# Kernel tuning notes

Hardware: AMD Instinct MI355X
Metric: run time of the kernel (lower is better)

## Reference

```python
import jax, jax.numpy as jnp
import numpy as np
from jax import lax

B, C, H, W = 16, 256, 80, 80
MID = 64
BN_EPS = 1e-5

SOBEL_X = jnp.array([[-1., 0., 1.], [-2., 0., 2.], [-1., 0., 1.]], jnp.float32) / 8.0
SOBEL_Y = jnp.array([[-1., -2., -1.], [0., 0., 0.], [1., 2., 1.]], jnp.float32) / 8.0
HAAR_LH = jnp.array([[1., -1.], [1., -1.]], jnp.float32) / 2.0
HAAR_HL = jnp.array([[1., 1.], [-1., -1.]], jnp.float32) / 2.0

DN = ('NCHW', 'OIHW', 'NCHW')

def dwconv(x, k2d, pad):
    # depthwise conv: same 2d kernel applied to every channel independently
    c = x.shape[1]
    k = jnp.broadcast_to(k2d[None, None], (c, 1) + k2d.shape)
    return lax.conv_general_dilated(x, k, (1, 1), [(pad, pad), (pad, pad)],
                                    dimension_numbers=DN, feature_group_count=c)

def avg_pool5(x):
    # matches F.avg_pool2d(k=5, s=1, p=2) with count_include_pad=True (divide by 25 always)
    s = lax.reduce_window(x, 0.0, lax.add, (1, 1, 5, 5), (1, 1, 1, 1),
                          [(0, 0), (0, 0), (2, 2), (2, 2)])
    return s / 25.0

def local_variance(x):
    m = avg_pool5(x)
    msq = avg_pool5(x * x)
    return jnp.clip(msq - m * m, 0.0, None)

def bn_silu(x, g, b, m, v):
    # inference batchnorm + SiLU, per-channel params over dim 1
    scale = (g / jnp.sqrt(v + BN_EPS))[None, :, None, None]
    shift = (b - m * g / jnp.sqrt(v + BN_EPS))[None, :, None, None]
    return jax.nn.silu(x * scale + shift)

def setup_inputs() -> dict:
    key = jax.random.key(0)
    ks = jax.random.split(key, 12)
    return {
        'x': jax.random.normal(ks[0], (B, C, H, W), jnp.float32),
        'proj_w': jax.random.normal(ks[1], (MID, C), jnp.float32) * 0.05,
        'bn1_g': jax.random.uniform(ks[2], (MID,), jnp.float32),
        'bn1_b': jax.random.normal(ks[3], (MID,), jnp.float32) * 0.1,
        'bn1_m': jax.random.normal(ks[4], (MID,), jnp.float32) * 0.1,
        'bn1_v': jax.random.uniform(ks[5], (MID,), jnp.float32) + 0.5,
        'fuse1_w': jax.random.normal(ks[6], (MID, MID + 2, 3, 3), jnp.float32) * 0.05,
        'bn2_g': jax.random.uniform(ks[7], (MID,), jnp.float32),
        'bn2_b': jax.random.normal(ks[8], (MID,), jnp.float32) * 0.1,
        'bn2_m': jax.random.normal(ks[9], (MID,), jnp.float32) * 0.1,
        'bn2_v': jax.random.uniform(ks[10], (MID,), jnp.float32) + 0.5,
        'fuse2_w': jax.random.normal(ks[11], (1, MID), jnp.float32) * 0.1,
    }

def reference(x, proj_w, bn1_g, bn1_b, bn1_m, bn1_v,
              fuse1_w, bn2_g, bn2_b, bn2_m, bn2_v, fuse2_w):
    b, c, h, w = x.shape
    # --- edge density ---
    gx = dwconv(x, SOBEL_X, 1)
    gy = dwconv(x, SOBEL_Y, 1)
    edge = jnp.sqrt(gx * gx + gy * gy).mean(axis=1, keepdims=True)  # (B,1,H,W)
    edge_density = edge / (avg_pool5(edge) + 1e-6)
    # --- periodicity ---
    lh = dwconv(x, HAAR_LH, 0)  # (B,C,H-1,W-1)
    hl = dwconv(x, HAAR_HL, 0)
    lh = jax.image.resize(lh, (b, c, h, w), method='bilinear')  # half-pixel, matches align_corners=False
    hl = jax.image.resize(hl, (b, c, h, w), method='bilinear')
    period = jnp.sqrt(local_variance(lh) + local_variance(hl) + 1e-6).mean(axis=1, keepdims=True)
    # --- feat_proj: 1x1 conv + BN + SiLU ---
    feat = bn_silu(jnp.einsum('bchw,mc->bmhw', x, proj_w), bn1_g, bn1_b, bn1_m, bn1_v)
    # --- fuse: 3x3 conv + BN + SiLU -> 1x1 conv -> sigmoid ---
    combined = jnp.concatenate([feat, edge_density, period], axis=1)  # (B,MID+2,H,W)
    y = lax.conv_general_dilated(combined, fuse1_w, (1, 1), [(1, 1), (1, 1)], dimension_numbers=DN)
    y = bn_silu(y, bn2_g, bn2_b, bn2_m, bn2_v)
    weight = jax.nn.sigmoid(jnp.einsum('bmhw,om->bohw', y, fuse2_w))  # (B,1,H,W)
    return x * weight
```

## Files before the change

### kernel.cpp

```cpp
#include <hip/hip_runtime.h>
#include <hip/hip_bf16.h>
#include <math.h>

#define HWN 6400
#define CC 256
#define MIDN 64

typedef _Float16 f16x8 __attribute__((ext_vector_type(8)));
typedef _Float16 f16x4 __attribute__((ext_vector_type(4)));
typedef _Float16 h2    __attribute__((ext_vector_type(2)));
typedef float    f32x4 __attribute__((ext_vector_type(4)));
typedef int      i32x4 __attribute__((ext_vector_type(4)));
typedef unsigned short u16;

__device__ __forceinline__ h2 pk2(float a, float b) {
    return __builtin_bit_cast(h2, __builtin_amdgcn_cvt_pkrtz(a, b));
}
__device__ __forceinline__ float h2lo(h2 v) { return (float)v[0]; }
__device__ __forceinline__ float h2hi(h2 v) { return (float)v[1]; }
__device__ __forceinline__ unsigned h2u(h2 v) { return __builtin_bit_cast(unsigned, v); }
__device__ __forceinline__ h2 u2h(unsigned u) { return __builtin_bit_cast(h2, u); }
__device__ __forceinline__ float u16f(u16 v) { return (float)__builtin_bit_cast(_Float16, v); }
__device__ __forceinline__ float vsqrtf_(float x) { float r; asm("v_sqrt_f32 %0, %1" : "=v"(r) : "v"(x)); return r; }

__global__ void prep_kernel(const float* __restrict__ proj_w,
                            const float* __restrict__ g1, const float* __restrict__ b1,
                            const float* __restrict__ m1, const float* __restrict__ v1,
                            const float* __restrict__ f1w,
                            const float* __restrict__ g2, const float* __restrict__ b2,
                            const float* __restrict__ m2, const float* __restrict__ v2,
                            _Float16* __restrict__ apack_proj,
                            _Float16* __restrict__ apack_fuse,
                            float* __restrict__ bias1, float* __restrict__ bias2) {
    int gid = blockIdx.x * blockDim.x + threadIdx.x;
    int stride = gridDim.x * blockDim.x;
    if (gid < MIDN) {
        float s1 = g1[gid] * rsqrtf(v1[gid] + 1e-5f);
        bias1[gid] = b1[gid] - m1[gid] * s1;
        float s2 = g2[gid] * rsqrtf(v2[gid] + 1e-5f);
        bias2[gid] = b2[gid] - m2[gid] * s2;
    }
    for (int i = gid; i < 8 * 4 * 64 * 8; i += stride) {
        int j = i & 7, lane = (i >> 3) & 63, w = (i >> 9) & 3, c = i >> 11;
        int m = w * 16 + (lane & 15);
        int ch = c * 32 + (lane >> 4) * 8 + j;
        float s1 = g1[m] * rsqrtf(v1[m] + 1e-5f);
        apack_proj[i] = (_Float16)(proj_w[m * CC + ch] * s1);
    }
    for (int i = gid; i < 9 * 3 * 4 * 64 * 8; i += stride) {
        int j = i & 7, lane = (i >> 3) & 63, w = (i >> 9) & 3;
        int tc = i >> 11; int c = tc % 3, t = tc / 3;
        int m = w * 16 + (lane & 15);
        int ch = c * 32 + (lane >> 4) * 8 + j;
        float s2 = g2[m] * rsqrtf(v2[m] + 1e-5f);
        float v = 0.f;
        if (ch < 66) v = f1w[(m * 66 + ch) * 9 + t] * s2;
        apack_fuse[i] = (_Float16)v;
    }
}

__launch_bounds__(256, 4)
__global__ void edge_period_pc_kernel(const float* __restrict__ x,
                                      u16* __restrict__ part_e,
                                      u16* __restrict__ part_p) {
    __shared__ unsigned wb[4][88];
    volatile unsigned (*wbv)[88] = wb;
    int tid = threadIdx.x;
    int w = tid >> 6, l = tid & 63;
    int b = blockIdx.y, cg = blockIdx.x;
    int row0 = w * 20;
    int im1 = (l + 63) & 63, ip1 = (l + 1) & 63;
    bool is0 = (l == 0), is63 = (l == 63), isB = (l < 16);

    if (l < 4) wbv[w][(l < 2) ? l : 80 + l] = 0u;

    float cwA = (l <= 0) ? 1.f : ((l >= 79) ? 0.f : (0.99375f - 0.0125f * (float)l));
    int cB = 64 + l;
    float cwB = (cB >= 79) ? 0.f : (0.99375f - 0.0125f * (float)cB);
    h2 v_pk = pk2(0.5f * cwA, 0.5f * cwB);
    h2 u_pk = pk2(0.5f * (1.f - cwA), 0.5f * (1.f - cwB));

    const float* xch = x + ((size_t)(b * CC + cg)) * HWN;
    u16* pe = part_e + ((size_t)(cg * 16 + b)) * HWN;
    u16* pp = part_p + ((size_t)(cg * 16 + b)) * HWN;

    auto rawload = [&](int rr) -> h2 {
        float a = 0.f, bb = 0.f;
        if (rr >= 0 && rr < 80) {
            a = xch[rr * 80 + l];
            if (isB) bb = xch[rr * 80 + 64 + l];
        }
        return pk2(a, bb);
    };
    auto mktrip = [&](h2 xc, h2& t0, h2& t2) {
        int xi = __builtin_bit_cast(int, xc);
        unsigned um = (unsigned)__shfl(xi, im1);
        unsigned up = (unsigned)__shfl(xi, ip1);
        um = is0 ? ((um & 0xFFFFu) << 16) : um;
        up = is63 ? (up >> 16) : up;
        t0 = u2h(um); t2 = u2h(up);
    };
    h2 xm1_0, xm1_1, xm1_2, x0_0, x0_1, x0_2, xp1_0, xp1_1, xp1_2;
    h2 rh, nh;
    nh = rawload(row0 - 3);
    rh = rawload(row0 - 2);
    xm1_1 = nh; mktrip(nh, xm1_0, xm1_2);
    x0_1 = rh;  mktrip(rh, x0_0, x0_2);
    rh = rawload(row0 - 1);
    h2 lhc_p, hlc_p;
    {
        h2 sa = xm1_0 + x0_0, sb = xm1_1 + x0_1, sc2 = xm1_2 + x0_2;
        h2 da = xm1_0 - x0_0, db = xm1_1 - x0_1, dc = xm1_2 - x0_2;
        lhc_p = u_pk * (sa - sb) + v_pk * (sb - sc2);
        hlc_p = u_pk * (da + db) + v_pk * (db + dc);
    }
    h2 ringA[5], ringB[5], ringS[5];
#pragma unroll
    for (int s = 0; s < 24; s++) {
        int r = row0 - 2 + s;
        if (s < 23) nh = rawload(row0 + s);
        xp1_1 = rh; mktrip(rh, xp1_0, xp1_2);
        if (s >= 2 && s < 22) {
            h2 gx = (xm1_2 - xm1_0) + (x0_2 - x0_0) + (x0_2 - x0_0) + (xp1_2 - xp1_0);
            h2 gy = (xp1_0 - xm1_0) + (xp1_1 - xm1_1) + (xp1_1 - xm1_1) + (xp1_2 - xm1_2);
            h2 g2v = gx * gx + gy * gy;
            unsigned eu = h2u(pk2(vsqrtf_(h2lo(g2v)) * 0.125f, vsqrtf_(h2hi(g2v)) * 0.125f));
            pe[r * 80 + l] = (u16)(eu & 0xFFFFu);
            if (isB) pe[r * 80 + 64 + l] = (u16)(eu >> 16);
        }
        h2 sa = x0_0 + xp1_0, sb = x0_1 + xp1_1, sc2 = x0_2 + xp1_2;
        h2 da = x0_0 - xp1_0, db = x0_1 - xp1_1, dc = x0_2 - xp1_2;
        h2 lhc = u_pk * (sa - sb) + v_pk * (sb - sc2);
        h2 hlc = u_pk * (da + db) + v_pk * (db + dc);
        float cw = (r <= 0) ? 1.f : ((r >= 79) ? 0.f : (0.99375f - 0.0125f * (float)r));
        h2 cwp = pk2(cw, cw), pwp = pk2(1.f - cw, 1.f - cw);
        h2 lhr = pwp * lhc_p + cwp * lhc;
        h2 hlr = pwp * hlc_p + cwp * hlc;
        lhc_p = lhc; hlc_p = hlc;
        unsigned lu = h2u(lhr), hu = h2u(hlr);
        unsigned fA = (lu & 0xFFFFu) | (hu << 16);
        unsigned fB = (lu >> 16) | (hu & 0xFFFF0000u);
        bool fv = (r >= 0) && (r < 80);
        if (!fv) { fA = 0u; fB = 0u; }
        wbv[w][2 + l] = fA;
        if (isB) wbv[w][66 + l] = fB;
        unsigned am2 = wbv[w][l], am1 = wbv[w][l + 1], ap1 = wbv[w][l + 3], ap2 = wbv[w][l + 4];
        unsigned bm2 = 0, bm1 = 0, bp1 = 0, bp2 = 0;
        if (isB) { bm2 = wbv[w][64 + l]; bm1 = wbv[w][65 + l]; bp1 = wbv[w][67 + l]; bp2 = wbv[w][68 + l]; }
        h2 fAh = u2h(fA), fBh = u2h(fB);
        h2 n0 = u2h(am2), n1 = u2h(am1), n2 = u2h(ap1), n3 = u2h(ap2);
        h2 hA = fAh + n0 + n1 + n2 + n3;
        h2 qa = fAh * fAh + n0 * n0 + n1 * n1 + n2 * n2 + n3 * n3;
        float s2A = h2lo(qa) + h2hi(qa);
        h2 m0 = u2h(bm2), m1 = u2h(bm1), m2 = u2h(bp1), m3 = u2h(bp2);
        h2 hB = fBh + m0 + m1 + m2 + m3;
        h2 qb = fBh * fBh + m0 * m0 + m1 * m1 + m2 * m2 + m3 * m3;
        float s2B = h2lo(qb) + h2hi(qb);
        ringA[s % 5] = hA; ringB[s % 5] = hB;
        ringS[s % 5] = pk2(s2A, s2B);
        if (s >= 4) {
            h2 SA = ringA[0] + ringA[1] + ringA[2] + ringA[3] + ringA[4];
            h2 SB = ringB[0] + ringB[1] + ringB[2] + ringB[3] + ringB[4];
            h2 S2 = ringS[0] + ringS[1] + ringS[2] + ringS[3] + ringS[4];
            float SLA = h2lo(SA), SHA = h2hi(SA);
            float SLB = h2lo(SB), SHB = h2hi(SB);
            float vA = 0.04f * h2lo(S2) - 0.0016f * (SLA * SLA + SHA * SHA);
            float vB = 0.04f * h2hi(S2) - 0.0016f * (SLB * SLB + SHB * SHB);
            vA = fmaxf(vA, 0.f) + 1e-6f;
            vB = fmaxf(vB, 0.f) + 1e-6f;
            unsigned pu = h2u(pk2(vsqrtf_(vA), vsqrtf_(vB)));
            int orow = row0 + s - 4;
            pp[orow * 80 + l] = (u16)(pu & 0xFFFFu);
            if (isB) pp[orow * 80 + 64 + l] = (u16)(pu >> 16);
        }
        xm1_0 = x0_0; xm1_1 = x0_1; xm1_2 = x0_2;
        x0_0 = xp1_0; x0_1 = xp1_1; x0_2 = xp1_2;
        rh = nh;
    }
}

#define NCGB 64
__launch_bounds__(512, 4)
__global__ void edge_period_acc_kernel(const float* __restrict__ x,
                                       u16* __restrict__ part_e,
                                       u16* __restrict__ part_p) {
    __shared__ unsigned wb[8][88];
    volatile unsigned (*wbv)[88] = wb;
    int tid = threadIdx.x;
    int w = tid >> 6, l = tid & 63;
    int b = blockIdx.y, cg = blockIdx.x;
    int row0 = w * 10;
    int im1 = (l + 63) & 63, ip1 = (l + 1) & 63;
    bool is0 = (l == 0), is63 = (l == 63), isB = (l < 16);

    if (l < 4) wbv[w][(l < 2) ? l : 80 + l] = 0u;

    float cwA = (l <= 0) ? 1.f : ((l >= 79) ? 0.f : (0.99375f - 0.0125f * (float)l));
    int cB = 64 + l;
    float cwB = (cB >= 79) ? 0.f : (0.99375f - 0.0125f * (float)cB);
    h2 v_pk = pk2(0.5f * cwA, 0.5f * cwB);
    h2 u_pk = pk2(0.5f * (1.f - cwA), 0.5f * (1.f - cwB));

    h2 erh[10], prh[10];
#pragma unroll
    for (int k = 0; k < 10; k++) { erh[k] = u2h(0u); prh[k] = u2h(0u); }

#pragma unroll 1
    for (int ch = 0; ch < 4; ch++) {
        const float* xch = x + ((size_t)(b * CC + cg * 4 + ch)) * HWN;
        auto rawload = [&](int rr) -> h2 {
            float a = 0.f, bb = 0.f;
            if (rr >= 0 && rr < 80) {
                a = xch[rr * 80 + l];
                if (isB) bb = xch[rr * 80 + 64 + l];
            }
            return pk2(a, bb);
        };
        auto mktrip = [&](h2 xc, h2& t0, h2& t2) {
            int xi = __builtin_bit_cast(int, xc);
            unsigned um = (unsigned)__shfl(xi, im1);
            unsigned up = (unsigned)__shfl(xi, ip1);
            um = is0 ? ((um & 0xFFFFu) << 16) : um;
            up = is63 ? (up >> 16) : up;
            t0 = u2h(um); t2 = u2h(up);
        };
        h2 xm1_0, xm1_1, xm1_2, x0_0, x0_1, x0_2, xp1_0, xp1_1, xp1_2;
        h2 rh, nh;
        nh = rawload(row0 - 3);
        rh = rawload(row0 - 2);
        xm1_1 = nh; mktrip(nh, xm1_0, xm1_2);
        x0_1 = rh;  mktrip(rh, x0_0, x0_2);
        rh = rawload(row0 - 1);
        h2 lhc_p, hlc_p;
        {
            h2 sa = xm1_0 + x0_0, sb = xm1_1 + x0_1, sc2 = xm1_2 + x0_2;
            h2 da = xm1_0 - x0_0, db = xm1_1 - x0_1, dc = xm1_2 - x0_2;
            lhc_p = u_pk * (sa - sb) + v_pk * (sb - sc2);
            hlc_p = u_pk * (da + db) + v_pk * (db + dc);
        }
        h2 ringA[5], ringB[5], ringS[5];
#pragma unroll
        for (int s = 0; s < 14; s++) {
            int r = row0 - 2 + s;
            if (s < 13) nh = rawload(row0 + s);
            xp1_1 = rh; mktrip(rh, xp1_0, xp1_2);
            if (s >= 2 && s < 12) {
                h2 gx = (xm1_2 - xm1_0) + (x0_2 - x0_0) + (x0_2 - x0_0) + (xp1_2 - xp1_0);
                h2 gy = (xp1_0 - xm1_0) + (xp1_1 - xm1_1) + (xp1_1 - xm1_1) + (xp1_2 - xm1_2);
                h2 g2v = gx * gx + gy * gy;
                erh[s - 2] += pk2(vsqrtf_(h2lo(g2v)) * 0.125f, vsqrtf_(h2hi(g2v)) * 0.125f);
            }
            h2 sa = x0_0 + xp1_0, sb = x0_1 + xp1_1, sc2 = x0_2 + xp1_2;
            h2 da = x0_0 - xp1_0, db = x0_1 - xp1_1, dc = x0_2 - xp1_2;
            h2 lhc = u_pk * (sa - sb) + v_pk * (sb - sc2);
            h2 hlc = u_pk * (da + db) + v_pk * (db + dc);
            float cw = (r <= 0) ? 1.f : ((r >= 79) ? 0.f : (0.99375f - 0.0125f * (float)r));
            h2 cwp = pk2(cw, cw), pwp = pk2(1.f - cw, 1.f - cw);
            h2 lhr = pwp * lhc_p + cwp * lhc;
            h2 hlr = pwp * hlc_p + cwp * hlc;
            lhc_p = lhc; hlc_p = hlc;
            unsigned lu = h2u(lhr), hu = h2u(hlr);
            unsigned fA = (lu & 0xFFFFu) | (hu << 16);
            unsigned fB = (lu >> 16) | (hu & 0xFFFF0000u);
            bool fv = (r >= 0) && (r < 80);
            if (!fv) { fA = 0u; fB = 0u; }
            wbv[w][2 + l] = fA;
            if (isB) wbv[w][66 + l] = fB;
            unsigned am2 = wbv[w][l], am1 = wbv[w][l + 1], ap1 = wbv[w][l + 3], ap2 = wbv[w][l + 4];
            unsigned bm2 = 0, bm1 = 0, bp1 = 0, bp2 = 0;
            if (isB) { bm2 = wbv[w][64 + l]; bm1 = wbv[w][65 + l]; bp1 = wbv[w][67 + l]; bp2 = wbv[w][68 + l]; }
            h2 fAh = u2h(fA), fBh = u2h(fB);
            h2 n0 = u2h(am2), n1 = u2h(am1), n2 = u2h(ap1), n3 = u2h(ap2);
            h2 hA = fAh + n0 + n1 + n2 + n3;
            h2 qa = fAh * fAh + n0 * n0 + n1 * n1 + n2 * n2 + n3 * n3;
            float s2A = h2lo(qa) + h2hi(qa);
            h2 m0 = u2h(bm2), m1 = u2h(bm1), m2 = u2h(bp1), m3 = u2h(bp2);
            h2 hB = fBh + m0 + m1 + m2 + m3;
            h2 qb = fBh * fBh + m0 * m0 + m1 * m1 + m2 * m2 + m3 * m3;
            float s2B = h2lo(qb) + h2hi(qb);
            ringA[s % 5] = hA; ringB[s % 5] = hB;
            ringS[s % 5] = pk2(s2A, s2B);
            if (s >= 4) {
                h2 SA = ringA[0] + ringA[1] + ringA[2] + ringA[3] + ringA[4];
                h2 SB = ringB[0] + ringB[1] + ringB[2] + ringB[3] + ringB[4];
                h2 S2 = ringS[0] + ringS[1] + ringS[2] + ringS[3] + ringS[4];
                float SLA = h2lo(SA), SHA = h2hi(SA);
                float SLB = h2lo(SB), SHB = h2hi(SB);
                float vA = 0.04f * h2lo(S2) - 0.0016f * (SLA * SLA + SHA * SHA);
                float vB = 0.04f * h2hi(S2) - 0.0016f * (SLB * SLB + SHB * SHB);
                vA = fmaxf(vA, 0.f) + 1e-6f;
                vB = fmaxf(vB, 0.f) + 1e-6f;
                prh[s - 4] += pk2(vsqrtf_(vA), vsqrtf_(vB));
            }
            xm1_0 = x0_0; xm1_1 = x0_1; xm1_2 = x0_2;
            x0_0 = xp1_0; x0_1 = xp1_1; x0_2 = xp1_2;
            rh = nh;
        }
    }
    size_t base = ((size_t)(cg * 16 + b) * 80 + row0) * 80;
#pragma unroll
    for (int k = 0; k < 10; k++) {
        unsigned eu = h2u(erh[k]), pu = h2u(prh[k]);
        part_e[base + k * 80 + l] = (u16)(eu & 0xFFFFu);
        part_p[base + k * 80 + l] = (u16)(pu & 0xFFFFu);
        if (isB) {
            part_e[base + k * 80 + 64 + l] = (u16)(eu >> 16);
            part_p[base + k * 80 + 64 + l] = (u16)(pu >> 16);
        }
    }
}

__launch_bounds__(256)
__global__ void chsum_kernel(const u16* __restrict__ part_e,
                             const u16* __restrict__ part_p,
                             float* __restrict__ esum, float* __restrict__ psum,
                             int ngroups) {
    int b = blockIdx.y;
    int p = blockIdx.x * 256 + threadIdx.x;
    float e = 0.f, pp = 0.f;
#pragma unroll 8
    for (int g = 0; g < ngroups; g++) {
        size_t off = ((size_t)(g * 16 + b)) * HWN + p;
        e += u16f(part_e[off]);
        pp += u16f(part_p[off]);
    }
    esum[b * HWN + p] = e;
    psum[b * HWN + p] = pp;
}

__launch_bounds__(256)
__global__ void density_kernel(const float* __restrict__ esum,
                               const float* __restrict__ psum,
                               _Float16* __restrict__ feat_t) {
    __shared__ float E[14][84];
    __shared__ float Hs[14][84];
    __shared__ float Ps[10][80];
    int band = blockIdx.x, b = blockIdx.y, tid = threadIdx.x;
    int r0 = band * 10;
    if (tid < 56) { int rr = tid >> 2, c4 = tid & 3; E[rr][(c4 < 2) ? c4 : 80 + c4] = 0.f; }
    for (int idx = tid; idx < 14 * 80; idx += 256) {
        int rr = idx / 80, j = idx - rr * 80;
        int row = r0 - 2 + rr;
        float e = 0.f, p = 0.f;
        if (row >= 0 && row < 80) {
            size_t off = (size_t)b * HWN + row * 80 + j;
            e = esum[off]; p = psum[off];
        }
        E[rr][2 + j] = e * (1.f / 256.f);
        if (rr >= 2 && rr < 12) Ps[rr - 2][j] = p * (1.f / 256.f);
    }
    __syncthreads();
    for (int idx = tid; idx < 14 * 80; idx += 256) {
        int rr = idx / 80, j = idx - rr * 80;
        Hs[rr][2 + j] = E[rr][j] + E[rr][j + 1] + E[rr][j + 2] + E[rr][j + 3] + E[rr][j + 4];
    }
    __syncthreads();
    for (int idx = tid; idx < 10 * 80; idx += 256) {
        int k = idx / 80, j = idx - k * 80;
        int rr = k + 2;
        float pool = Hs[rr - 2][2 + j] + Hs[rr - 1][2 + j] + Hs[rr][2 + j]
                   + Hs[rr + 1][2 + j] + Hs[rr + 2][2 + j];
        float ed = E[rr][2 + j] / (pool * 0.04f + 1e-6f);
        _Float16* fp = feat_t + ((size_t)(b * HWN) + (r0 + k) * 80 + j) * 96;
        f16x8 z8 = {};
        f16x8 f8 = {};
        f8[0] = (_Float16)ed; f8[1] = (_Float16)Ps[k][j];
        *reinterpret_cast<f16x8*>(fp + 64) = f8;
        *reinterpret_cast<f16x8*>(fp + 72) = z8;
        *reinterpret_cast<f16x8*>(fp + 80) = z8;
        *reinterpret_cast<f16x8*>(fp + 88) = z8;
    }
}

__launch_bounds__(256)
__global__ void proj_kernel(const float* __restrict__ x,
                            const _Float16* __restrict__ apack,
                            const float* __restrict__ bias1,
                            _Float16* __restrict__ feat_t) {
    __shared__ __align__(16) unsigned char lds[64 * 512];
    int b = blockIdx.y, p0 = blockIdx.x * 64;
    int tid = threadIdx.x, w = tid >> 6, l = tid & 63;

#pragma unroll 4
    for (int i = 0; i < 16; i++) {
        int ch0 = i * 16 + w * 4;
        f16x4 v4;
#pragma unroll
        for (int q = 0; q < 4; q++)
            v4[q] = (_Float16)x[((size_t)(b * CC + ch0 + q)) * HWN + p0 + l];
        int byte = l * 512 + ((ch0 * 2) ^ ((l & 7) << 4));
        *reinterpret_cast<f16x4*>(lds + byte) = v4;
    }
    __syncthreads();

    const f16x8* Ap = reinterpret_cast<const f16x8*>(apack);
    f32x4 acc[4];
#pragma unroll
    for (int ct = 0; ct < 4; ct++) acc[ct] = (f32x4){0.f, 0.f, 0.f, 0.f};

    int kb = 16 * (l >> 4);
#pragma unroll 2
    for (int c = 0; c < 8; c++) {
        f16x8 a = Ap[(c * 4 + w) * 64 + l];
#pragma unroll
        for (int ct = 0; ct < 4; ct++) {
            int byte = (ct * 16 + (l & 15)) * 512 + ((c * 64 + kb) ^ ((l & 7) << 4));
            f16x8 bv = *reinterpret_cast<const f16x8*>(lds + byte);
            acc[ct] = __builtin_amdgcn_mfma_f32_16x16x32_f16(a, bv, acc[ct], 0, 0, 0);
        }
    }

    float b1v[4];
#pragma unroll
    for (int q = 0; q < 4; q++) b1v[q] = bias1[w * 16 + (l >> 4) * 4 + q];
#pragma unroll
    for (int ct = 0; ct < 4; ct++) {
        f16x4 o4;
#pragma unroll
        for (int q = 0; q < 4; q++) {
            float z = acc[ct][q] + b1v[q];
            o4[q] = (_Float16)(z / (1.f + expf(-z)));
        }
        size_t px = (size_t)(b * HWN) + p0 + ct * 16 + (l & 15);
        *reinterpret_cast<f16x4*>(feat_t + px * 96 + w * 16 + (l >> 4) * 4) = o4;
    }
}

#define TROW 256
__launch_bounds__(256)
__global__ void fuse_kernel(const _Float16* __restrict__ feat_t,
                            const _Float16* __restrict__ apack,
                            const float* __restrict__ bias2,
                            const float* __restrict__ fuse2,
                            const float* __restrict__ x,
                            float* __restrict__ out) {
    __shared__ __align__(16) unsigned char tl[108 * TROW];
    __shared__ float R[4 * 4 * 4 * 16];
    __shared__ float wgtbuf[64];
    int b = blockIdx.y, t5 = blockIdx.x;
    int ti = t5 / 5, tj = t5 - ti * 5;
    int i0 = ti * 4, j0 = tj * 16;
    int tid = threadIdx.x, w = tid >> 6, l = tid & 63;

    for (int idx = tid; idx < 1296; idx += 256) {
        int hpx = idx / 12, g = idx - hpx * 12;
        int hr = hpx / 18, hc = hpx - hr * 18;
        int gi = i0 - 1 + hr, gj = j0 - 1 + hc;
        i32x4 val = {0, 0, 0, 0};
        if (gi >= 0 && gi < 80 && gj >= 0 && gj < 80) {
            val = *reinterpret_cast<const i32x4*>(
                feat_t + ((size_t)(b * HWN) + gi * 80 + gj) * 96 + g * 8);
        }
        *reinterpret_cast<i32x4*>(tl + hpx * TROW + ((g * 16) ^ ((hc & 7) << 4))) = val;
    }
    __syncthreads();

    const f16x8* Ap = reinterpret_cast<const f16x8*>(apack);
    f32x4 acc[4];
#pragma unroll
    for (int r = 0; r < 4; r++) acc[r] = (f32x4){0.f, 0.f, 0.f, 0.f};
    int kb = 16 * (l >> 4);

#pragma unroll 1
    for (int t = 0; t < 9; t++) {
        int dy = t / 3, dx = t - dy * 3;
        f16x8 a0 = Ap[((t * 3 + 0) * 4 + w) * 64 + l];
        f16x8 a1 = Ap[((t * 3 + 1) * 4 + w) * 64 + l];
        f16x8 a2 = Ap[((t * 3 + 2) * 4 + w) * 64 + l];
        int hc = (l & 15) + dx;
        int key = (hc & 7) << 4;
#pragma unroll
        for (int r = 0; r < 4; r++) {
            int base = ((r + dy) * 18 + hc) * TROW;
            f16x8 b0 = *reinterpret_cast<const f16x8*>(tl + base + ((0 + kb) ^ key));
            acc[r] = __builtin_amdgcn_mfma_f32_16x16x32_f16(a0, b0, acc[r], 0, 0, 0);
            f16x8 b1_ = *reinterpret_cast<const f16x8*>(tl + base + ((64 + kb) ^ key));
            acc[r] = __builtin_amdgcn_mfma_f32_16x16x32_f16(a1, b1_, acc[r], 0, 0, 0);
            f16x8 b2_ = *reinterpret_cast<const f16x8*>(tl + base + ((128 + kb) ^ key));
            acc[r] = __builtin_amdgcn_mfma_f32_16x16x32_f16(a2, b2_, acc[r], 0, 0, 0);
        }
    }

    float b2v[4], f2v[4];
#pragma unroll
    for (int q = 0; q < 4; q++) {
        int m = w * 16 + (l >> 4) * 4 + q;
        b2v[q] = bias2[m];
        f2v[q] = fuse2[m];
    }
#pragma unroll
    for (int r = 0; r < 4; r++) {
        float p = 0.f;
#pragma unroll
        for (int q = 0; q < 4; q++) {
            float z = acc[r][q] + b2v[q];
            p += f2v[q] * (z / (1.f + expf(-z)));
        }
        R[((w * 4 + r) * 4 + (l >> 4)) * 16 + (l & 15)] = p;
    }
    __syncthreads();
    if (tid < 64) {
        int r = tid >> 4, cc = tid & 15;
        float s = 0.f;
#pragma unroll
        for (int w2 = 0; w2 < 4; w2++)
#pragma unroll
            for (int g2 = 0; g2 < 4; g2++)
                s += R[((w2 * 4 + r) * 4 + g2) * 16 + cc];
        wgtbuf[tid] = 1.f / (1.f + expf(-s));
    }
    __syncthreads();

    int r = l >> 4, cc = l & 15;
    float wgt = wgtbuf[l];
    size_t base = (size_t)b * CC * HWN + (size_t)((i0 + r) * 80 + j0 + cc);
    const float* xp = x + base;
    float* op = out + base;
#pragma unroll 4
    for (int ch = w * 64; ch < w * 64 + 64; ch++) {
        op[(size_t)ch * HWN] = xp[(size_t)ch * HWN] * wgt;
    }
}

extern "C" void kernel_launch(void* const* d_in, const int* in_sizes, int n_in,
                              void* d_out, int out_size, void* d_ws, size_t ws_size,
                              hipStream_t stream) {
    (void)in_sizes; (void)n_in; (void)out_size;
    const float* x       = (const float*)d_in[0];
    const float* proj_w  = (const float*)d_in[1];
    const float* bn1_g   = (const float*)d_in[2];
    const float* bn1_b   = (const float*)d_in[3];
    const float* bn1_m   = (const float*)d_in[4];
    const float* bn1_v   = (const float*)d_in[5];
    const float* fuse1_w = (const float*)d_in[6];
    const float* bn2_g   = (const float*)d_in[7];
    const float* bn2_b   = (const float*)d_in[8];
    const float* bn2_m   = (const float*)d_in[9];
    const float* bn2_v   = (const float*)d_in[10];
    const float* fuse2_w = (const float*)d_in[11];
    float* out = (float*)d_out;

    const size_t needA = (size_t)(256 * 16 * HWN) * 4
                       + (size_t)2 * 16 * HWN * 4
                       + (size_t)16 * HWN * 96 * 2
                       + (16384 + 55296) * 2 + 1024;
    bool useA = ws_size >= needA;
    int ngroups = useA ? 256 : NCGB;

    float* ws = (float*)d_ws;
    size_t partN = (size_t)ngroups * 16 * HWN;
    u16*      part_e      = (u16*)ws;
    u16*      part_p      = part_e + partN;
    float*    esum        = (float*)(part_p + partN);
    float*    psum        = esum + 16 * HWN;
    _Float16* feat_t      = (_Float16*)(psum + 16 * HWN);
    float*    after_feat  = (float*)(feat_t + (size_t)16 * HWN * 96);
    _Float16* apack_proj  = (_Float16*)after_feat;
    _Float16* apack_fuse  = apack_proj + 16384;
    float*    bias1       = (float*)(apack_fuse + 55296);
    float*    bias2       = bias1 + 64;

    prep_kernel<<<288, 256, 0, stream>>>(proj_w, bn1_g, bn1_b, bn1_m, bn1_v,
                                         fuse1_w, bn2_g, bn2_b, bn2_m, bn2_v,
                                         apack_proj, apack_fuse, bias1, bias2);
    if (useA) {
        edge_period_pc_kernel<<<dim3(256, 16), 256, 0, stream>>>(x, part_e, part_p);
    } else {
        edge_period_acc_kernel<<<dim3(NCGB, 16), 512, 0, stream>>>(x, part_e, part_p);
    }
    chsum_kernel<<<dim3(25, 16), 256, 0, stream>>>(part_e, part_p, esum, psum, ngroups);
    density_kernel<<<dim3(8, 16), 256, 0, stream>>>(esum, psum, feat_t);
    proj_kernel<<<dim3(100, 16), 256, 0, stream>>>(x, apack_proj, bias1, feat_t);
    fuse_kernel<<<dim3(100, 16), 256, 0, stream>>>(feat_t, apack_fuse,
                                                   bias2, fuse2_w, x, out);
}
```

Baseline: 224.1 us.

## Interleave edge and period partials per row and recompute top-row neighbour shuffles

Merges the separate edge and period partial buffers into one buffer where each row holds the 80 edge values followed by the 80 period values. Both the producer kernels and the channel-sum kernel are updated, so the reader fetches both quantities from nearby addresses. The xm1 neighbour values are no longer kept in registers and are rebuilt with extra shuffles when needed, which trades more shuffle instructions for lower register pressure. The reader's index math is slightly more complex, and locality between the two reads improves.

Result: faster. 218.1 us (-2.7%).

```diff
diff --git a/kernel.cpp b/kernel.cpp
--- a/kernel.cpp
+++ b/kernel.cpp
@@ -61,8 +61,7 @@
 
 __launch_bounds__(256, 4)
 __global__ void edge_period_pc_kernel(const float* __restrict__ x,
-                                      u16* __restrict__ part_e,
-                                      u16* __restrict__ part_p) {
+                                      u16* __restrict__ part) {
     __shared__ unsigned wb[4][88];
     volatile unsigned (*wbv)[88] = wb;
     int tid = threadIdx.x;
@@ -81,8 +80,7 @@
     h2 u_pk = pk2(0.5f * (1.f - cwA), 0.5f * (1.f - cwB));
 
     const float* xch = x + ((size_t)(b * CC + cg)) * HWN;
-    u16* pe = part_e + ((size_t)(cg * 16 + b)) * HWN;
-    u16* pp = part_p + ((size_t)(cg * 16 + b)) * HWN;
+    u16* pout = part + ((size_t)(cg * 16 + b)) * (HWN * 2);
 
     auto rawload = [&](int rr) -> h2 {
         float a = 0.f, bb = 0.f;
@@ -92,7 +90,7 @@
         }
         return pk2(a, bb);
     };
-    auto mktrip = [&](h2 xc, h2& t0, h2& t2) {
+    auto nbrs = [&](h2 xc, h2& t0, h2& t2) {
         int xi = __builtin_bit_cast(int, xc);
         unsigned um = (unsigned)__shfl(xi, im1);
         unsigned up = (unsigned)__shfl(xi, ip1);
@@ -100,17 +98,19 @@
         up = is63 ? (up >> 16) : up;
         t0 = u2h(um); t2 = u2h(up);
     };
-    h2 xm1_0, xm1_1, xm1_2, x0_0, x0_1, x0_2, xp1_0, xp1_1, xp1_2;
+    h2 xm1_1, x0_0, x0_1, x0_2, xp1_0, xp1_1, xp1_2;
     h2 rh, nh;
     nh = rawload(row0 - 3);
     rh = rawload(row0 - 2);
-    xm1_1 = nh; mktrip(nh, xm1_0, xm1_2);
-    x0_1 = rh;  mktrip(rh, x0_0, x0_2);
+    xm1_1 = nh;
+    x0_1 = rh; nbrs(rh, x0_0, x0_2);
     rh = rawload(row0 - 1);
     h2 lhc_p, hlc_p;
     {
-        h2 sa = xm1_0 + x0_0, sb = xm1_1 + x0_1, sc2 = xm1_2 + x0_2;
-        h2 da = xm1_0 - x0_0, db = xm1_1 - x0_1, dc = xm1_2 - x0_2;
+        h2 m0, m2;
+        nbrs(xm1_1, m0, m2);
+        h2 sa = m0 + x0_0, sb = xm1_1 + x0_1, sc2 = m2 + x0_2;
+        h2 da = m0 - x0_0, db = xm1_1 - x0_1, dc = m2 - x0_2;
         lhc_p = u_pk * (sa - sb) + v_pk * (sb - sc2);
         hlc_p = u_pk * (da + db) + v_pk * (db + dc);
     }
@@ -119,14 +119,16 @@
     for (int s = 0; s < 24; s++) {
         int r = row0 - 2 + s;
         if (s < 23) nh = rawload(row0 + s);
-        xp1_1 = rh; mktrip(rh, xp1_0, xp1_2);
+        xp1_1 = rh; nbrs(rh, xp1_0, xp1_2);
         if (s >= 2 && s < 22) {
-            h2 gx = (xm1_2 - xm1_0) + (x0_2 - x0_0) + (x0_2 - x0_0) + (xp1_2 - xp1_0);
-            h2 gy = (xp1_0 - xm1_0) + (xp1_1 - xm1_1) + (xp1_1 - xm1_1) + (xp1_2 - xm1_2);
+            h2 m0, m2;
+            nbrs(xm1_1, m0, m2);
+            h2 gx = (m2 - m0) + (x0_2 - x0_0) + (x0_2 - x0_0) + (xp1_2 - xp1_0);
+            h2 gy = (xp1_0 - m0) + (xp1_1 - xm1_1) + (xp1_1 - xm1_1) + (xp1_2 - m2);
             h2 g2v = gx * gx + gy * gy;
             unsigned eu = h2u(pk2(vsqrtf_(h2lo(g2v)) * 0.125f, vsqrtf_(h2hi(g2v)) * 0.125f));
-            pe[r * 80 + l] = (u16)(eu & 0xFFFFu);
-            if (isB) pe[r * 80 + 64 + l] = (u16)(eu >> 16);
+            pout[r * 160 + l] = (u16)(eu & 0xFFFFu);
+            if (isB) pout[r * 160 + 64 + l] = (u16)(eu >> 16);
         }
         h2 sa = x0_0 + xp1_0, sb = x0_1 + xp1_1, sc2 = x0_2 + xp1_2;
         h2 da = x0_0 - xp1_0, db = x0_1 - xp1_1, dc = x0_2 - xp1_2;
@@ -152,9 +154,9 @@
         h2 hA = fAh + n0 + n1 + n2 + n3;
         h2 qa = fAh * fAh + n0 * n0 + n1 * n1 + n2 * n2 + n3 * n3;
         float s2A = h2lo(qa) + h2hi(qa);
-        h2 m0 = u2h(bm2), m1 = u2h(bm1), m2 = u2h(bp1), m3 = u2h(bp2);
-        h2 hB = fBh + m0 + m1 + m2 + m3;
-        h2 qb = fBh * fBh + m0 * m0 + m1 * m1 + m2 * m2 + m3 * m3;
+        h2 m0q = u2h(bm2), m1q = u2h(bm1), m2q = u2h(bp1), m3q = u2h(bp2);
+        h2 hB = fBh + m0q + m1q + m2q + m3q;
+        h2 qb = fBh * fBh + m0q * m0q + m1q * m1q + m2q * m2q + m3q * m3q;
         float s2B = h2lo(qb) + h2hi(qb);
         ringA[s % 5] = hA; ringB[s % 5] = hB;
         ringS[s % 5] = pk2(s2A, s2B);
@@ -170,10 +172,10 @@
             vB = fmaxf(vB, 0.f) + 1e-6f;
             unsigned pu = h2u(pk2(vsqrtf_(vA), vsqrtf_(vB)));
             int orow = row0 + s - 4;
-            pp[orow * 80 + l] = (u16)(pu & 0xFFFFu);
-            if (isB) pp[orow * 80 + 64 + l] = (u16)(pu >> 16);
-        }
-        xm1_0 = x0_0; xm1_1 = x0_1; xm1_2 = x0_2;
+            pout[orow * 160 + 80 + l] = (u16)(pu & 0xFFFFu);
+            if (isB) pout[orow * 160 + 144 + l] = (u16)(pu >> 16);
+        }
+        xm1_1 = x0_1;
         x0_0 = xp1_0; x0_1 = xp1_1; x0_2 = xp1_2;
         rh = nh;
     }
@@ -182,8 +184,7 @@
 #define NCGB 64
 __launch_bounds__(512, 4)
 __global__ void edge_period_acc_kernel(const float* __restrict__ x,
-                                       u16* __restrict__ part_e,
-                                       u16* __restrict__ part_p) {
+                                       u16* __restrict__ part) {
     __shared__ unsigned wb[8][88];
     volatile unsigned (*wbv)[88] = wb;
     int tid = threadIdx.x;
@@ -216,7 +217,7 @@
             }
             return pk2(a, bb);
         };
-        auto mktrip = [&](h2 xc, h2& t0, h2& t2) {
+        auto nbrs = [&](h2 xc, h2& t0, h2& t2) {
             int xi = __builtin_bit_cast(int, xc);
             unsigned um = (unsigned)__shfl(xi, im1);
             unsigned up = (unsigned)__shfl(xi, ip1);
@@ -224,17 +225,19 @@
             up = is63 ? (up >> 16) : up;
             t0 = u2h(um); t2 = u2h(up);
         };
-        h2 xm1_0, xm1_1, xm1_2, x0_0, x0_1, x0_2, xp1_0, xp1_1, xp1_2;
+        h2 xm1_1, x0_0, x0_1, x0_2, xp1_0, xp1_1, xp1_2;
         h2 rh, nh;
         nh = rawload(row0 - 3);
         rh = rawload(row0 - 2);
-        xm1_1 = nh; mktrip(nh, xm1_0, xm1_2);
-        x0_1 = rh;  mktrip(rh, x0_0, x0_2);
+        xm1_1 = nh;
+        x0_1 = rh; nbrs(rh, x0_0, x0_2);
         rh = rawload(row0 - 1);
         h2 lhc_p, hlc_p;
         {
-            h2 sa = xm1_0 + x0_0, sb = xm1_1 + x0_1, sc2 = xm1_2 + x0_2;
-            h2 da = xm1_0 - x0_0, db = xm1_1 - x0_1, dc = xm1_2 - x0_2;
+            h2 m0, m2;
+            nbrs(xm1_1, m0, m2);
+            h2 sa = m0 + x0_0, sb = xm1_1 + x0_1, sc2 = m2 + x0_2;
+            h2 da = m0 - x0_0, db = xm1_1 - x0_1, dc = m2 - x0_2;
             lhc_p = u_pk * (sa - sb) + v_pk * (sb - sc2);
             hlc_p = u_pk * (da + db) + v_pk * (db + dc);
         }
@@ -243,10 +246,12 @@
         for (int s = 0; s < 14; s++) {
             int r = row0 - 2 + s;
             if (s < 13) nh = rawload(row0 + s);
-            xp1_1 = rh; mktrip(rh, xp1_0, xp1_2);
+            xp1_1 = rh; nbrs(rh, xp1_0, xp1_2);
             if (s >= 2 && s < 12) {
-                h2 gx = (xm1_2 - xm1_0) + (x0_2 - x0_0) + (x0_2 - x0_0) + (xp1_2 - xp1_0);
-                h2 gy = (xp1_0 - xm1_0) + (xp1_1 - xm1_1) + (xp1_1 - xm1_1) + (xp1_2 - xm1_2);
+                h2 m0, m2;
+                nbrs(xm1_1, m0, m2);
+                h2 gx = (m2 - m0) + (x0_2 - x0_0) + (x0_2 - x0_0) + (xp1_2 - xp1_0);
+                h2 gy = (xp1_0 - m0) + (xp1_1 - xm1_1) + (xp1_1 - xm1_1) + (xp1_2 - m2);
                 h2 g2v = gx * gx + gy * gy;
                 erh[s - 2] += pk2(vsqrtf_(h2lo(g2v)) * 0.125f, vsqrtf_(h2hi(g2v)) * 0.125f);
             }
@@ -274,9 +279,9 @@
             h2 hA = fAh + n0 + n1 + n2 + n3;
             h2 qa = fAh * fAh + n0 * n0 + n1 * n1 + n2 * n2 + n3 * n3;
             float s2A = h2lo(qa) + h2hi(qa);
-            h2 m0 = u2h(bm2), m1 = u2h(bm1), m2 = u2h(bp1), m3 = u2h(bp2);
-            h2 hB = fBh + m0 + m1 + m2 + m3;
-            h2 qb = fBh * fBh + m0 * m0 + m1 * m1 + m2 * m2 + m3 * m3;
+            h2 m0q = u2h(bm2), m1q = u2h(bm1), m2q = u2h(bp1), m3q = u2h(bp2);
+            h2 hB = fBh + m0q + m1q + m2q + m3q;
+            h2 qb = fBh * fBh + m0q * m0q + m1q * m1q + m2q * m2q + m3q * m3q;
             float s2B = h2lo(qb) + h2hi(qb);
             ringA[s % 5] = hA; ringB[s % 5] = hB;
             ringS[s % 5] = pk2(s2A, s2B);
@@ -292,37 +297,38 @@
                 vB = fmaxf(vB, 0.f) + 1e-6f;
                 prh[s - 4] += pk2(vsqrtf_(vA), vsqrtf_(vB));
             }
-            xm1_0 = x0_0; xm1_1 = x0_1; xm1_2 = x0_2;
+            xm1_1 = x0_1;
             x0_0 = xp1_0; x0_1 = xp1_1; x0_2 = xp1_2;
             rh = nh;
         }
     }
-    size_t base = ((size_t)(cg * 16 + b) * 80 + row0) * 80;
+    size_t base = ((size_t)(cg * 16 + b)) * (HWN * 2);
 #pragma unroll
     for (int k = 0; k < 10; k++) {
+        int row = row0 + k;
         unsigned eu = h2u(erh[k]), pu = h2u(prh[k]);
-        part_e[base + k * 80 + l] = (u16)(eu & 0xFFFFu);
-        part_p[base + k * 80 + l] = (u16)(pu & 0xFFFFu);
+        part[base + row * 160 + l] = (u16)(eu & 0xFFFFu);
+        part[base + row * 160 + 80 + l] = (u16)(pu & 0xFFFFu);
         if (isB) {
-            part_e[base + k * 80 + 64 + l] = (u16)(eu >> 16);
-            part_p[base + k * 80 + 64 + l] = (u16)(pu >> 16);
+            part[base + row * 160 + 64 + l] = (u16)(eu >> 16);
+            part[base + row * 160 + 144 + l] = (u16)(pu >> 16);
         }
     }
 }
 
 __launch_bounds__(256)
-__global__ void chsum_kernel(const u16* __restrict__ part_e,
-                             const u16* __restrict__ part_p,
+__global__ void chsum_kernel(const u16* __restrict__ part,
                              float* __restrict__ esum, float* __restrict__ psum,
                              int ngroups) {
     int b = blockIdx.y;
     int p = blockIdx.x * 256 + threadIdx.x;
+    int row = p / 80, j = p - row * 80;
     float e = 0.f, pp = 0.f;
 #pragma unroll 8
     for (int g = 0; g < ngroups; g++) {
-        size_t off = ((size_t)(g * 16 + b)) * HWN + p;
-        e += u16f(part_e[off]);
-        pp += u16f(part_p[off]);
+        size_t off = ((size_t)(g * 16 + b)) * (HWN * 2) + row * 160 + j;
+        e += u16f(part[off]);
+        pp += u16f(part[off + 80]);
     }
     esum[b * HWN + p] = e;
     psum[b * HWN + p] = pp;
@@ -548,10 +554,9 @@
     int ngroups = useA ? 256 : NCGB;
 
     float* ws = (float*)d_ws;
-    size_t partN = (size_t)ngroups * 16 * HWN;
-    u16*      part_e      = (u16*)ws;
-    u16*      part_p      = part_e + partN;
-    float*    esum        = (float*)(part_p + partN);
+    size_t partN = (size_t)ngroups * 16 * HWN * 2;
+    u16*      part        = (u16*)ws;
+    float*    esum        = (float*)(part + partN);
     float*    psum        = esum + 16 * HWN;
     _Float16* feat_t      = (_Float16*)(psum + 16 * HWN);
     float*    after_feat  = (float*)(feat_t + (size_t)16 * HWN * 96);
@@ -564,11 +569,11 @@
                                          fuse1_w, bn2_g, bn2_b, bn2_m, bn2_v,
                                          apack_proj, apack_fuse, bias1, bias2);
     if (useA) {
-        edge_period_pc_kernel<<<dim3(256, 16), 256, 0, stream>>>(x, part_e, part_p);
+        edge_period_pc_kernel<<<dim3(256, 16), 256, 0, stream>>>(x, part);
     } else {
-        edge_period_acc_kernel<<<dim3(NCGB, 16), 512, 0, stream>>>(x, part_e, part_p);
-    }
-    chsum_kernel<<<dim3(25, 16), 256, 0, stream>>>(part_e, part_p, esum, psum, ngroups);
+        edge_period_acc_kernel<<<dim3(NCGB, 16), 512, 0, stream>>>(x, part);
+    }
+    chsum_kernel<<<dim3(25, 16), 256, 0, stream>>>(part, esum, psum, ngroups);
     density_kernel<<<dim3(8, 16), 256, 0, stream>>>(esum, psum, feat_t);
     proj_kernel<<<dim3(100, 16), 256, 0, stream>>>(x, apack_proj, bias1, feat_t);
     fuse_kernel<<<dim3(100, 16), 256, 0, stream>>>(feat_t, apack_fuse,
```
